# Kernel optimization log

Hardware: AMD Instinct MI355X
Metric: run time of the kernel (lower is better)

## Reference

```python
import jax, jax.numpy as jnp
import numpy as np
import math

B, L, D, H, TOPK = 2, 2048, 1024, 16, 5
DK = D // H
U = min(TOPK * int(np.ceil(np.log1p(L))), L)  # = 40 selected queries


def setup_inputs() -> dict:
    k = jax.random.key(0)
    ks = jax.random.split(k, 9)
    s = 1.0 / math.sqrt(D)  # ~ torch Linear init scale
    return {
        "query": jax.random.normal(ks[0], (B, L, D), jnp.float32),
        "key": jax.random.normal(ks[1], (B, L, D), jnp.float32),
        "value": jax.random.normal(ks[2], (B, L, D), jnp.float32),
        "Wq": jax.random.uniform(ks[3], (D, D), jnp.float32, -s, s),
        "bq": jax.random.uniform(ks[4], (D,), jnp.float32, -s, s),
        "Wk": jax.random.uniform(ks[5], (D, D), jnp.float32, -s, s),
        "bk": jax.random.uniform(ks[6], (D,), jnp.float32, -s, s),
        "Wv": jax.random.uniform(ks[7], (D, D), jnp.float32, -s, s),
        "bv": jax.random.uniform(ks[8], (D,), jnp.float32, -s, s),
    }


def reference(query, key, value, Wq, bq, Wk, bk, Wv, bv):
    # torch Linear: y = x @ W.T + b ; split_heads -> [B, H, L, DK]
    def split(x):
        return x.reshape(B, L, H, DK).transpose(0, 2, 1, 3)

    Q = split(query @ Wq.T + bq)
    K = split(key @ Wk.T + bk)
    V = split(value @ Wv.T + bv)

    # Full score matrix [B,H,L,L]; used only for the sparsity measure M
    # (original's Q_K_sample actually uses full K; sampling is dead code).
    scores_full = jnp.einsum('bhqd,bhkd->bhqk', Q, K)
    M = scores_full.max(axis=-1) - scores_full.mean(axis=-1)  # [B,H,L]

    _, M_top = jax.lax.top_k(M, U)  # [B,H,U] (torch uses sorted=False; set identical)

    Q_red = jnp.take_along_axis(Q, M_top[..., None], axis=2)  # [B,H,U,DK]
    attn_scores = jnp.einsum('bhqd,bhkd->bhqk', Q_red, K) / math.sqrt(DK)

    # default causal mask rows gathered at the selected query positions
    causal = jnp.triu(jnp.ones((L, L), jnp.float32), 1)  # [L_Q, L_K]
    attn_scores = attn_scores + causal[M_top] * (-1e9)   # [B,H,U,L]

    attn_probs = jax.nn.softmax(attn_scores, axis=-1)
    attn = jnp.einsum('bhql,bhld->bqhd', attn_probs, V).reshape(B, U, D)
    return attn, attn_probs
```

## Files before the change

### kernel.cpp

```cpp
#include <hip/hip_runtime.h>
#include <hip/hip_bf16.h>

#define BB 2
#define LL 2048
#define DD 1024
#define HH 16
#define DK 64
#define UU 40
#define BH (BB*HH)

typedef unsigned short u16;
typedef float f32x4 __attribute__((ext_vector_type(4)));
typedef short s16x8 __attribute__((ext_vector_type(8)));

__device__ inline float b2f_r8(u16 x) {
    union { unsigned short u; __hip_bfloat16 b; } c; c.u = x;
    return __bfloat162float(c.b);
}
__device__ inline float ldf_r8(const void* p, size_t i, int isF) {
    return isF ? ((const float*)p)[i] : b2f_r8(((const u16*)p)[i]);
}
__device__ inline f32x4 ld4_r8(const void* p, size_t i, int isF) {
    if (isF) return *(const f32x4*)((const float*)p + i);
    ushort4 v = *(const ushort4*)((const u16*)p + i);
    f32x4 r;
    r[0] = b2f_r8(v.x); r[1] = b2f_r8(v.y); r[2] = b2f_r8(v.z); r[3] = b2f_r8(v.w);
    return r;
}
__device__ inline void cvt2_r8(float x, u16& h, u16& l) {
    union { __hip_bfloat16 b; u16 u; } ch, cl;
    ch.b = __float2bfloat16(x);
    float hf = __bfloat162float(ch.b);
    cl.b = __float2bfloat16(x - hf);
    h = ch.u; l = cl.u;
}

__global__ __launch_bounds__(256) void detect_dtype_r8(const u16* __restrict__ q,
                                                       int* __restrict__ flag) {
    __shared__ float red[256];
    int tid = threadIdx.x;
    float mx = 0.f;
    for (int i = tid; i < 4096; i += 256) {
        float v = fabsf(b2f_r8(q[i]));
        if (!(v < 1e30f)) v = 1e38f;
        mx = fmaxf(mx, v);
    }
    red[tid] = mx; __syncthreads();
    for (int s = 128; s > 0; s >>= 1) {
        if (tid < s) red[tid] = fmaxf(red[tid], red[tid + s]);
        __syncthreads();
    }
    if (tid == 0) *flag = (red[0] > 1e20f) ? 1 : 0;
}

#define PAD 132

__global__ __launch_bounds__(256) void proj_f4_r13(
    const void* __restrict__ key, const void* __restrict__ query,
    const void* __restrict__ Wk, const void* __restrict__ Wq,
    const void* __restrict__ bk, const void* __restrict__ bq,
    float* __restrict__ Kf, float* __restrict__ Qf,
    const int* __restrict__ flag)
{
    __shared__ float sX[32 * PAD];
    __shared__ float sW[32 * 68];
    int tid = threadIdx.x;
    int n0 = blockIdx.x * 128, f0 = blockIdx.y * 64, z = blockIdx.z;
    const void* X    = z ? query : key;
    const void* W    = z ? Wq    : Wk;
    const void* bias = z ? bq    : bk;
    float* out       = z ? Qf    : Kf;
    int isF = *flag;
    int tx = tid & 15, ty = tid >> 4;

    float acc[8][4];
#pragma unroll
    for (int a = 0; a < 8; ++a)
#pragma unroll
        for (int c = 0; c < 4; ++c) acc[a][c] = 0.f;

    for (int kc = 0; kc < 32; ++kc) {
        __syncthreads();
#pragma unroll
        for (int it = 0; it < 4; ++it) {
            int row = 64 * (it & 1) + (tid >> 2);
            int d4 = (tid & 3) | ((it >> 1) << 2);
            f32x4 v = ld4_r8(X, (size_t)(n0 + row) * DD + kc * 32 + d4 * 4, isF);
#pragma unroll
            for (int cc = 0; cc < 4; ++cc)
                sX[(4 * d4 + cc) * PAD + row] = v[cc];
        }
#pragma unroll
        for (int it = 0; it < 2; ++it) {
            int row = tid >> 2;
            int d4 = (tid & 3) | (it << 2);
            f32x4 v = ld4_r8(W, (size_t)(f0 + row) * DD + kc * 32 + d4 * 4, isF);
#pragma unroll
            for (int cc = 0; cc < 4; ++cc)
                sW[(4 * d4 + cc) * 68 + row] = v[cc];
        }
        __syncthreads();
        for (int d = 0; d < 32; ++d) {
            const f32x4 xa = *(const f32x4*)(&sX[d * PAD + ty * 4]);
            const f32x4 xb = *(const f32x4*)(&sX[d * PAD + 64 + ty * 4]);
            const f32x4 wa = *(const f32x4*)(&sW[d * 68 + tx * 4]);
            float xv[8] = {xa[0], xa[1], xa[2], xa[3], xb[0], xb[1], xb[2], xb[3]};
#pragma unroll
            for (int a = 0; a < 8; ++a)
#pragma unroll
                for (int c = 0; c < 4; ++c)
                    acc[a][c] = fmaf(xv[a], wa[c], acc[a][c]);
        }
    }
#pragma unroll
    for (int a = 0; a < 8; ++a) {
        int n = n0 + (a >> 2) * 64 + ty * 4 + (a & 3);
        int b = n >> 11, l = n & (LL - 1);
#pragma unroll
        for (int c = 0; c < 4; ++c) {
            int f = f0 + tx * 4 + c;
            int h = f >> 6, dk = f & 63;
            out[((size_t)(b * HH + h) * LL + l) * DK + dk] =
                acc[a][c] + ldf_r8(bias, (size_t)f, isF);
        }
    }
}

#define LDK 72
__global__ __launch_bounds__(256) void proj_mfma_v_r9(
    const void* __restrict__ X, const void* __restrict__ W,
    const void* __restrict__ bias, float* __restrict__ out,
    const int* __restrict__ flag)
{
    __shared__ u16 Ahi[128 * LDK];
    __shared__ u16 Alo[128 * LDK];
    __shared__ u16 Bhi[128 * LDK];
    __shared__ u16 Blo[128 * LDK];
    int tid = threadIdx.x;
    int n0 = blockIdx.x * 128, f0 = blockIdx.y * 128;
    int isF = *flag;
    int lane = tid & 63, w = tid >> 6, wr = w >> 1, wc = w & 1;

    f32x4 acc[4][4] = {};

    for (int kc = 0; kc < 16; ++kc) {
        __syncthreads();
#pragma unroll
        for (int it = 0; it < 16; ++it) {
            int i = it * 256 + tid;
            int isB = i >> 11, j = i & 2047;
            int row = j >> 4, c = (j & 15) << 2;
            f32x4 v = ld4_r8(isB ? W : X, (size_t)((isB ? f0 : n0) + row) * DD + kc * 64 + c, isF);
            u16* hh = isB ? Bhi : Ahi;
            u16* ll = isB ? Blo : Alo;
            ushort4 h4, l4;
            cvt2_r8(v[0], h4.x, l4.x);
            cvt2_r8(v[1], h4.y, l4.y);
            cvt2_r8(v[2], h4.z, l4.z);
            cvt2_r8(v[3], h4.w, l4.w);
            *(ushort4*)&hh[row * LDK + c] = h4;
            *(ushort4*)&ll[row * LDK + c] = l4;
        }
        __syncthreads();
#pragma unroll
        for (int kk = 0; kk < 2; ++kk) {
            int koff = kk * 32 + (lane >> 4) * 8;
            s16x8 ah[4], al[4];
#pragma unroll
            for (int mi = 0; mi < 4; ++mi) {
                int r = wr * 64 + mi * 16 + (lane & 15);
                ah[mi] = *(const s16x8*)&Ahi[r * LDK + koff];
                al[mi] = *(const s16x8*)&Alo[r * LDK + koff];
            }
#pragma unroll
            for (int ni = 0; ni < 4; ++ni) {
                int r = wc * 64 + ni * 16 + (lane & 15);
                s16x8 bh = *(const s16x8*)&Bhi[r * LDK + koff];
                s16x8 bl = *(const s16x8*)&Blo[r * LDK + koff];
#pragma unroll
                for (int mi = 0; mi < 4; ++mi) {
                    acc[mi][ni] = __builtin_amdgcn_mfma_f32_16x16x32_bf16(ah[mi], bh, acc[mi][ni], 0, 0, 0);
                    acc[mi][ni] = __builtin_amdgcn_mfma_f32_16x16x32_bf16(al[mi], bh, acc[mi][ni], 0, 0, 0);
                    acc[mi][ni] = __builtin_amdgcn_mfma_f32_16x16x32_bf16(ah[mi], bl, acc[mi][ni], 0, 0, 0);
                }
            }
        }
    }

#pragma unroll
    for (int ni = 0; ni < 4; ++ni) {
        int f = f0 + wc * 64 + ni * 16 + (lane & 15);
        float bb = ldf_r8(bias, (size_t)f, isF);
        int h = f >> 6, dk = f & 63;
#pragma unroll
        for (int mi = 0; mi < 4; ++mi) {
            int nbase = n0 + wr * 64 + mi * 16 + ((lane >> 4) << 2);
#pragma unroll
            for (int j2 = 0; j2 < 4; ++j2) {
                int n = nbase + j2, b = n >> 11, l = n & (LL - 1);
                out[((size_t)(b * HH + h) * LL + l) * DK + dk] = acc[mi][ni][j2] + bb;
            }
        }
    }
}

__global__ __launch_bounds__(256) void kbar_r8(
    const float* __restrict__ Kf, double* __restrict__ Kbar)
{
    __shared__ double red[256];
    int bh = blockIdx.x, tid = threadIdx.x;
    int d = tid & 63, seg = tid >> 6;
    double s = 0;
    for (int l = seg * 512; l < seg * 512 + 512; ++l)
        s += (double)Kf[((size_t)bh * LL + l) * DK + d];
    red[tid] = s; __syncthreads();
    if (tid < 128) red[tid] += red[tid + 128];
    __syncthreads();
    if (tid < 64) Kbar[(size_t)bh * DK + d] = (red[tid] + red[tid + 64]) * (1.0 / (double)LL);
}

#define QT 64
__global__ __launch_bounds__(256) void stats_max_r13(
    const float* __restrict__ Qf, const float* __restrict__ Kf,
    const double* __restrict__ Kbar, double* __restrict__ Mv)
{
    __shared__ float sQ[64 * 68];
    __shared__ float sK[64 * 68];
    __shared__ float rowmax[QT];
    int tid = threadIdx.x;
    int q0 = blockIdx.x * QT, bh = blockIdx.y;
    int tx = tid & 15, ty = tid >> 4;

    {
        const float* src = Qf + ((size_t)bh * LL + q0) * DK;
#pragma unroll
        for (int it = 0; it < 4; ++it) {
            int row = tid >> 2;
            int d4 = (tid & 3) | (it << 2);
            f32x4 v = *(const f32x4*)(src + (size_t)row * DK + d4 * 4);
#pragma unroll
            for (int cc = 0; cc < 4; ++cc)
                sQ[(4 * d4 + cc) * 68 + row] = v[cc];
        }
    }
    float rmax4[4];
#pragma unroll
    for (int a = 0; a < 4; ++a) rmax4[a] = -INFINITY;

    const float* kbase = Kf + (size_t)bh * LL * DK;
    for (int kc = 0; kc < 32; ++kc) {
        __syncthreads();
#pragma unroll
        for (int it = 0; it < 4; ++it) {
            int row = tid >> 2;
            int d4 = (tid & 3) | (it << 2);
            f32x4 v = *(const f32x4*)(kbase + (size_t)(kc * 64 + row) * DK + d4 * 4);
#pragma unroll
            for (int cc = 0; cc < 4; ++cc)
                sK[(4 * d4 + cc) * 68 + row] = v[cc];
        }
        __syncthreads();
        float acc[4][4];
#pragma unroll
        for (int a = 0; a < 4; ++a)
#pragma unroll
            for (int c = 0; c < 4; ++c) acc[a][c] = 0.f;
        for (int d = 0; d < 64; ++d) {
            const f32x4 qa = *(const f32x4*)(&sQ[d * 68 + ty * 4]);
            const f32x4 ka = *(const f32x4*)(&sK[d * 68 + tx * 4]);
#pragma unroll
            for (int a = 0; a < 4; ++a)
#pragma unroll
                for (int c = 0; c < 4; ++c)
                    acc[a][c] = fmaf(qa[a], ka[c], acc[a][c]);
        }
#pragma unroll
        for (int a = 0; a < 4; ++a)
#pragma unroll
            for (int c = 0; c < 4; ++c) rmax4[a] = fmaxf(rmax4[a], acc[a][c]);
    }
#pragma unroll
    for (int a = 0; a < 4; ++a) {
        float v = rmax4[a];
        v = fmaxf(v, __shfl_xor(v, 1));
        v = fmaxf(v, __shfl_xor(v, 2));
        v = fmaxf(v, __shfl_xor(v, 4));
        v = fmaxf(v, __shfl_xor(v, 8));
        rmax4[a] = v;
    }
    if (tx == 0) {
#pragma unroll
        for (int a = 0; a < 4; ++a)
            rowmax[ty * 4 + a] = rmax4[a];
    }
    __syncthreads();
    if (tid < QT) {
        const double* kb = Kbar + (size_t)bh * DK;
        double s = 0;
#pragma unroll
        for (int d = 0; d < 64; ++d) s += (double)sQ[d * 68 + tid] * kb[d];
        Mv[(size_t)bh * LL + q0 + tid] = (double)rowmax[tid] - s;
    }
}

__global__ __launch_bounds__(64) void topk_wave_r10(
    const double* __restrict__ Mv, int* __restrict__ sel)
{
    int bh = blockIdx.x, lane = threadIdx.x;
    double v[32];
#pragma unroll
    for (int t = 0; t < 32; ++t) v[t] = Mv[(size_t)bh * LL + t * 64 + lane];
    for (int u = 0; u < UU; ++u) {
        double bv = -1e301; int bi = LL;
#pragma unroll
        for (int t = 0; t < 32; ++t) {
            double x = v[t]; int j = t * 64 + lane;
            if (x > bv || (x == bv && j < bi)) { bv = x; bi = j; }
        }
#pragma unroll
        for (int off = 1; off < 64; off <<= 1) {
            double ov = __shfl_xor(bv, off); int oi = __shfl_xor(bi, off);
            if (ov > bv || (ov == bv && oi < bi)) { bv = ov; bi = oi; }
        }
        if ((bi & 63) == lane) {
            int ts = bi >> 6;
#pragma unroll
            for (int t = 0; t < 32; ++t)
                if (t == ts) v[t] = -1e302;
        }
        if (lane == 0) sel[bh * UU + u] = bi;
    }
}

__global__ __launch_bounds__(256) void scores_r15(
    const float* __restrict__ Qf, const float* __restrict__ Kf,
    const int* __restrict__ sel, float* __restrict__ S)
{
    __shared__ float sK[128 * 68];
    __shared__ float qsm[40 * 68];
    __shared__ int qpos[UU];
    int lq = blockIdx.x, bh = blockIdx.y, tid = threadIdx.x;
    int l0 = lq * 128;
    if (tid < UU) qpos[tid] = sel[bh * UU + tid];
    __syncthreads();
    for (int i = tid; i < 640; i += 256) {
        int u = i >> 4, c4 = i & 15;
        *(f32x4*)&qsm[u * 68 + c4 * 4] =
            *(const f32x4*)&Qf[((size_t)bh * LL + qpos[u]) * DK + c4 * 4];
    }
#pragma unroll
    for (int it = 0; it < 8; ++it) {
        int idx = it * 256 + tid;
        int l = idx >> 4, d4 = idx & 15;
        *(f32x4*)&sK[l * 68 + d4 * 4] =
            *(const f32x4*)&Kf[((size_t)bh * LL + l0 + l) * DK + d4 * 4];
    }
    __syncthreads();
    int gu = tid >> 5, lt = tid & 31;
    float acc[5][4];
#pragma unroll
    for (int ui = 0; ui < 5; ++ui)
#pragma unroll
        for (int li = 0; li < 4; ++li) acc[ui][li] = 0.f;
    for (int d16 = 0; d16 < 16; ++d16) {
        f32x4 qf[5], kf[4];
#pragma unroll
        for (int ui = 0; ui < 5; ++ui)
            qf[ui] = *(const f32x4*)&qsm[(gu + 8 * ui) * 68 + d16 * 4];
#pragma unroll
        for (int li = 0; li < 4; ++li)
            kf[li] = *(const f32x4*)&sK[(lt + 32 * li) * 68 + d16 * 4];
#pragma unroll
        for (int ui = 0; ui < 5; ++ui)
#pragma unroll
            for (int li = 0; li < 4; ++li)
#pragma unroll
                for (int c = 0; c < 4; ++c)
                    acc[ui][li] = fmaf(qf[ui][c], kf[li][c], acc[ui][li]);
    }
#pragma unroll
    for (int ui = 0; ui < 5; ++ui) {
        int u = gu + 8 * ui;
        int qp = qpos[u];
#pragma unroll
        for (int li = 0; li < 4; ++li) {
            int l = l0 + lt + 32 * li;
            float s = acc[ui][li] * 0.125f;
            if (l > qp) s -= 1e9f;
            S[((size_t)bh * UU + u) * LL + l] = s;
        }
    }
}

__global__ __launch_bounds__(256) void softmax_r12(
    const float* __restrict__ S, float* __restrict__ probsOut)
{
    __shared__ float red[256];
    int u = blockIdx.x, bh = blockIdx.y, tid = threadIdx.x;
    size_t rowo = ((size_t)bh * UU + u) * LL;
    float sloc[8];
    float lmax = -INFINITY;
#pragma unroll
    for (int c = 0; c < 8; ++c) {
        sloc[c] = S[rowo + c * 256 + tid];
        lmax = fmaxf(lmax, sloc[c]);
    }
    red[tid] = lmax; __syncthreads();
    for (int s2 = 128; s2 > 0; s2 >>= 1) {
        if (tid < s2) red[tid] = fmaxf(red[tid], red[tid + s2]);
        __syncthreads();
    }
    float mval = red[0];
    __syncthreads();
    float lsum = 0.f;
#pragma unroll
    for (int c = 0; c < 8; ++c) { sloc[c] = expf(sloc[c] - mval); lsum += sloc[c]; }
    red[tid] = lsum; __syncthreads();
    for (int s2 = 128; s2 > 0; s2 >>= 1) {
        if (tid < s2) red[tid] += red[tid + s2];
        __syncthreads();
    }
    float inv = 1.0f / red[0];
#pragma unroll
    for (int c = 0; c < 8; ++c)
        probsOut[rowo + c * 256 + tid] = sloc[c] * inv;
}

__global__ __launch_bounds__(256) void pv_r15(
    const float* __restrict__ probsOut, const float* __restrict__ Vf,
    float* __restrict__ part)
{
    __shared__ float pP[20 * 256];
    int lq = blockIdx.x, bh = blockIdx.y, ug2 = blockIdx.z, tid = threadIdx.x;
    int l0 = lq * 256;
#pragma unroll
    for (int it = 0; it < 5; ++it) {
        int idx = it * 256 + tid;
        int ur = idx >> 6, l4 = idx & 63;
        *(f32x4*)&pP[ur * 256 + l4 * 4] =
            *(const f32x4*)&probsOut[((size_t)bh * UU + ug2 * 20 + ur) * LL + l0 + l4 * 4];
    }
    __syncthreads();
    int dk = tid & 63, ug = tid >> 6;
    const float* vb = Vf + ((size_t)bh * LL + l0) * DK + dk;
    float acc[5];
#pragma unroll
    for (int j = 0; j < 5; ++j) acc[j] = 0.f;
    for (int l4 = 0; l4 < 64; ++l4) {
        float vv0 = vb[(size_t)(l4 * 4 + 0) * DK];
        float vv1 = vb[(size_t)(l4 * 4 + 1) * DK];
        float vv2 = vb[(size_t)(l4 * 4 + 2) * DK];
        float vv3 = vb[(size_t)(l4 * 4 + 3) * DK];
#pragma unroll
        for (int j = 0; j < 5; ++j) {
            const f32x4 p4 = *(const f32x4*)&pP[(ug * 5 + j) * 256 + l4 * 4];
            acc[j] = fmaf(p4[0], vv0, acc[j]);
            acc[j] = fmaf(p4[1], vv1, acc[j]);
            acc[j] = fmaf(p4[2], vv2, acc[j]);
            acc[j] = fmaf(p4[3], vv3, acc[j]);
        }
    }
#pragma unroll
    for (int j = 0; j < 5; ++j) {
        int u = ug2 * 20 + ug * 5 + j;
        part[(((size_t)bh * 8 + lq) * UU + u) * DK + dk] = acc[j];
    }
}

__global__ __launch_bounds__(64) void pvred_r12(
    const float* __restrict__ part, float* __restrict__ attnOut)
{
    int u = blockIdx.x, bh = blockIdx.y, dk = threadIdx.x;
    int b = bh >> 4, h = bh & 15;
    float s = 0.f;
#pragma unroll
    for (int lq = 0; lq < 8; ++lq)
        s += part[(((size_t)bh * 8 + lq) * UU + u) * DK + dk];
    attnOut[((size_t)b * UU + u) * DD + h * DK + dk] = s;
}

extern "C" void kernel_launch(void* const* d_in, const int* in_sizes, int n_in,
                              void* d_out, int out_size, void* d_ws, size_t ws_size,
                              hipStream_t stream) {
    (void)in_sizes; (void)n_in; (void)out_size; (void)ws_size;
    const void* query = d_in[0];
    const void* key   = d_in[1];
    const void* value = d_in[2];
    const void* Wq    = d_in[3];
    const void* bq    = d_in[4];
    const void* Wk    = d_in[5];
    const void* bk    = d_in[6];
    const void* Wv    = d_in[7];
    const void* bv    = d_in[8];

    char* w = (char*)d_ws;
    const size_t NE = (size_t)BB * HH * LL * DK;
    float* Kf  = (float*)w;  w += NE * 4;
    float* Vf  = (float*)w;  w += NE * 4;
    float* Qf  = (float*)w;  w += NE * 4;
    double* Mv = (double*)w; w += (size_t)BH * LL * 8;
    double* Kbar = (double*)w; w += (size_t)BH * DK * 8;
    int* sel   = (int*)w;    w += (size_t)BH * UU * 4;
    int* flag  = (int*)w;    w += 64;
    float* S    = (float*)w; w += (size_t)BH * UU * LL * 4;
    float* part = (float*)w; w += (size_t)BH * 8 * UU * DK * 4;

    float* attnOut  = (float*)d_out;
    float* probsOut = attnOut + (size_t)BB * UU * DD;

    dim3 blk(256);
    detect_dtype_r8<<<1, blk, 0, stream>>>((const u16*)query, flag);
    proj_f4_r13<<<dim3(32, 16, 2), blk, 0, stream>>>(key, query, Wk, Wq, bk, bq,
                                                     Kf, Qf, flag);
    proj_mfma_v_r9<<<dim3(32, 8), blk, 0, stream>>>(value, Wv, bv, Vf, flag);
    kbar_r8<<<32, blk, 0, stream>>>(Kf, Kbar);
    stats_max_r13<<<dim3(LL / QT, 32), blk, 0, stream>>>(Qf, Kf, Kbar, Mv);
    topk_wave_r10<<<32, dim3(64), 0, stream>>>(Mv, sel);
    scores_r15<<<dim3(16, 32), blk, 0, stream>>>(Qf, Kf, sel, S);
    softmax_r12<<<dim3(UU, 32), blk, 0, stream>>>(S, probsOut);
    pv_r15<<<dim3(8, 32, 2), blk, 0, stream>>>(probsOut, Vf, part);
    pvred_r12<<<dim3(UU, 32), dim3(64), 0, stream>>>(part, attnOut);
}
```

Baseline: 912.2 us.

## Pre-convert Wv to bf16 hi/lo, shrink V-proj tile, enlarge stats query tile

```diff
diff --git a/kernel.cpp b/kernel.cpp
--- a/kernel.cpp
+++ b/kernel.cpp
@@ -126,49 +126,70 @@
     }
 }
 
+__global__ __launch_bounds__(256) void preconvW_r16(
+    const void* __restrict__ Wv, u16* __restrict__ Whi, u16* __restrict__ Wlo,
+    const int* __restrict__ flag)
+{
+    int isF = *flag;
+    size_t i = ((size_t)blockIdx.x * 256 + threadIdx.x) * 4;
+    f32x4 v = ld4_r8(Wv, i, isF);
+    ushort4 h4, l4;
+    cvt2_r8(v[0], h4.x, l4.x);
+    cvt2_r8(v[1], h4.y, l4.y);
+    cvt2_r8(v[2], h4.z, l4.z);
+    cvt2_r8(v[3], h4.w, l4.w);
+    *(ushort4*)&Whi[i] = h4;
+    *(ushort4*)&Wlo[i] = l4;
+}
+
 #define LDK 72
-__global__ __launch_bounds__(256) void proj_mfma_v_r9(
-    const void* __restrict__ X, const void* __restrict__ W,
-    const void* __restrict__ bias, float* __restrict__ out,
-    const int* __restrict__ flag)
-{
-    __shared__ u16 Ahi[128 * LDK];
-    __shared__ u16 Alo[128 * LDK];
+__global__ __launch_bounds__(256) void proj_mfma_v_r16(
+    const void* __restrict__ X, const u16* __restrict__ Whi,
+    const u16* __restrict__ Wlo, const void* __restrict__ bias,
+    float* __restrict__ out, const int* __restrict__ flag)
+{
+    __shared__ u16 Ahi[64 * LDK];
+    __shared__ u16 Alo[64 * LDK];
     __shared__ u16 Bhi[128 * LDK];
     __shared__ u16 Blo[128 * LDK];
     int tid = threadIdx.x;
-    int n0 = blockIdx.x * 128, f0 = blockIdx.y * 128;
+    int n0 = blockIdx.x * 64, f0 = blockIdx.y * 128;
     int isF = *flag;
     int lane = tid & 63, w = tid >> 6, wr = w >> 1, wc = w & 1;
 
-    f32x4 acc[4][4] = {};
+    f32x4 acc[2][4] = {};
 
     for (int kc = 0; kc < 16; ++kc) {
         __syncthreads();
 #pragma unroll
-        for (int it = 0; it < 16; ++it) {
+        for (int it = 0; it < 4; ++it) {
             int i = it * 256 + tid;
-            int isB = i >> 11, j = i & 2047;
-            int row = j >> 4, c = (j & 15) << 2;
-            f32x4 v = ld4_r8(isB ? W : X, (size_t)((isB ? f0 : n0) + row) * DD + kc * 64 + c, isF);
-            u16* hh = isB ? Bhi : Ahi;
-            u16* ll = isB ? Blo : Alo;
+            int row = i >> 4, c = (i & 15) << 2;
+            f32x4 v = ld4_r8(X, (size_t)(n0 + row) * DD + kc * 64 + c, isF);
             ushort4 h4, l4;
             cvt2_r8(v[0], h4.x, l4.x);
             cvt2_r8(v[1], h4.y, l4.y);
             cvt2_r8(v[2], h4.z, l4.z);
             cvt2_r8(v[3], h4.w, l4.w);
-            *(ushort4*)&hh[row * LDK + c] = h4;
-            *(ushort4*)&ll[row * LDK + c] = l4;
+            *(ushort4*)&Ahi[row * LDK + c] = h4;
+            *(ushort4*)&Alo[row * LDK + c] = l4;
+        }
+#pragma unroll
+        for (int it = 0; it < 8; ++it) {
+            int i = it * 256 + tid;
+            int row = i >> 4, c = (i & 15) << 2;
+            size_t go = (size_t)(f0 + row) * DD + kc * 64 + c;
+            *(ushort4*)&Bhi[row * LDK + c] = *(const ushort4*)&Whi[go];
+            *(ushort4*)&Blo[row * LDK + c] = *(const ushort4*)&Wlo[go];
         }
         __syncthreads();
 #pragma unroll
         for (int kk = 0; kk < 2; ++kk) {
             int koff = kk * 32 + (lane >> 4) * 8;
-            s16x8 ah[4], al[4];
-#pragma unroll
-            for (int mi = 0; mi < 4; ++mi) {
-                int r = wr * 64 + mi * 16 + (lane & 15);
+            s16x8 ah[2], al[2];
+#pragma unroll
+            for (int mi = 0; mi < 2; ++mi) {
+                int r = wr * 32 + mi * 16 + (lane & 15);
                 ah[mi] = *(const s16x8*)&Ahi[r * LDK + koff];
                 al[mi] = *(const s16x8*)&Alo[r * LDK + koff];
             }
@@ -178,7 +199,7 @@
                 s16x8 bh = *(const s16x8*)&Bhi[r * LDK + koff];
                 s16x8 bl = *(const s16x8*)&Blo[r * LDK + koff];
 #pragma unroll
-                for (int mi = 0; mi < 4; ++mi) {
+                for (int mi = 0; mi < 2; ++mi) {
                     acc[mi][ni] = __builtin_amdgcn_mfma_f32_16x16x32_bf16(ah[mi], bh, acc[mi][ni], 0, 0, 0);
                     acc[mi][ni] = __builtin_amdgcn_mfma_f32_16x16x32_bf16(al[mi], bh, acc[mi][ni], 0, 0, 0);
                     acc[mi][ni] = __builtin_amdgcn_mfma_f32_16x16x32_bf16(ah[mi], bl, acc[mi][ni], 0, 0, 0);
@@ -193,8 +214,8 @@
         float bb = ldf_r8(bias, (size_t)f, isF);
         int h = f >> 6, dk = f & 63;
 #pragma unroll
-        for (int mi = 0; mi < 4; ++mi) {
-            int nbase = n0 + wr * 64 + mi * 16 + ((lane >> 4) << 2);
+        for (int mi = 0; mi < 2; ++mi) {
+            int nbase = n0 + wr * 32 + mi * 16 + ((lane >> 4) << 2);
 #pragma unroll
             for (int j2 = 0; j2 < 4; ++j2) {
                 int n = nbase + j2, b = n >> 11, l = n & (LL - 1);
@@ -219,33 +240,33 @@
     if (tid < 64) Kbar[(size_t)bh * DK + d] = (red[tid] + red[tid + 64]) * (1.0 / (double)LL);
 }
 
-#define QT 64
-__global__ __launch_bounds__(256) void stats_max_r13(
+#define QTS 128
+__global__ __launch_bounds__(256) void stats_max_r12(
     const float* __restrict__ Qf, const float* __restrict__ Kf,
     const double* __restrict__ Kbar, double* __restrict__ Mv)
 {
-    __shared__ float sQ[64 * 68];
+    __shared__ float sQ[64 * PAD];
     __shared__ float sK[64 * 68];
-    __shared__ float rowmax[QT];
+    __shared__ float rowmax[QTS];
     int tid = threadIdx.x;
-    int q0 = blockIdx.x * QT, bh = blockIdx.y;
+    int q0 = blockIdx.x * QTS, bh = blockIdx.y;
     int tx = tid & 15, ty = tid >> 4;
 
     {
         const float* src = Qf + ((size_t)bh * LL + q0) * DK;
 #pragma unroll
-        for (int it = 0; it < 4; ++it) {
-            int row = tid >> 2;
-            int d4 = (tid & 3) | (it << 2);
+        for (int it = 0; it < 8; ++it) {
+            int row = 64 * (it & 1) + (tid >> 2);
+            int d4 = (tid & 3) | ((it >> 1) << 2);
             f32x4 v = *(const f32x4*)(src + (size_t)row * DK + d4 * 4);
 #pragma unroll
             for (int cc = 0; cc < 4; ++cc)
-                sQ[(4 * d4 + cc) * 68 + row] = v[cc];
-        }
-    }
-    float rmax4[4];
-#pragma unroll
-    for (int a = 0; a < 4; ++a) rmax4[a] = -INFINITY;
+                sQ[(4 * d4 + cc) * PAD + row] = v[cc];
+        }
+    }
+    float rmax8[8];
+#pragma unroll
+    for (int a = 0; a < 8; ++a) rmax8[a] = -INFINITY;
 
     const float* kbase = Kf + (size_t)bh * LL * DK;
     for (int kc = 0; kc < 32; ++kc) {
@@ -260,45 +281,49 @@
                 sK[(4 * d4 + cc) * 68 + row] = v[cc];
         }
         __syncthreads();
-        float acc[4][4];
-#pragma unroll
-        for (int a = 0; a < 4; ++a)
+        float acc[8][4];
+#pragma unroll
+        for (int a = 0; a < 8; ++a)
 #pragma unroll
             for (int c = 0; c < 4; ++c) acc[a][c] = 0.f;
         for (int d = 0; d < 64; ++d) {
-            const f32x4 qa = *(const f32x4*)(&sQ[d * 68 + ty * 4]);
+            const f32x4 qa = *(const f32x4*)(&sQ[d * PAD + ty * 4]);
+            const f32x4 qb = *(const f32x4*)(&sQ[d * PAD + 64 + ty * 4]);
             const f32x4 ka = *(const f32x4*)(&sK[d * 68 + tx * 4]);
-#pragma unroll
-            for (int a = 0; a < 4; ++a)
+            float qv[8] = {qa[0], qa[1], qa[2], qa[3], qb[0], qb[1], qb[2], qb[3]};
+#pragma unroll
+            for (int a = 0; a < 8; ++a)
 #pragma unroll
                 for (int c = 0; c < 4; ++c)
-                    acc[a][c] = fmaf(qa[a], ka[c], acc[a][c]);
-        }
-#pragma unroll
-        for (int a = 0; a < 4; ++a)
-#pragma unroll
-            for (int c = 0; c < 4; ++c) rmax4[a] = fmaxf(rmax4[a], acc[a][c]);
-    }
-#pragma unroll
-    for (int a = 0; a < 4; ++a) {
-        float v = rmax4[a];
+                    acc[a][c] = fmaf(qv[a], ka[c], acc[a][c]);
+        }
+#pragma unroll
+        for (int a = 0; a < 8; ++a)
+#pragma unroll
+            for (int c = 0; c < 4; ++c) rmax8[a] = fmaxf(rmax8[a], acc[a][c]);
+    }
+#pragma unroll
+    for (int a = 0; a < 8; ++a) {
+        float v = rmax8[a];
         v = fmaxf(v, __shfl_xor(v, 1));
         v = fmaxf(v, __shfl_xor(v, 2));
         v = fmaxf(v, __shfl_xor(v, 4));
         v = fmaxf(v, __shfl_xor(v, 8));
-        rmax4[a] = v;
+        rmax8[a] = v;
     }
     if (tx == 0) {
 #pragma unroll
-        for (int a = 0; a < 4; ++a)
-            rowmax[ty * 4 + a] = rmax4[a];
+        for (int a = 0; a < 8; ++a) {
+            int row = ty * 4 + (a & 3) + (a >> 2) * 64;
+            rowmax[row] = rmax8[a];
+        }
     }
     __syncthreads();
-    if (tid < QT) {
+    if (tid < QTS) {
         const double* kb = Kbar + (size_t)bh * DK;
         double s = 0;
 #pragma unroll
-        for (int d = 0; d < 64; ++d) s += (double)sQ[d * 68 + tid] * kb[d];
+        for (int d = 0; d < 64; ++d) s += (double)sQ[d * PAD + tid] * kb[d];
         Mv[(size_t)bh * LL + q0 + tid] = (double)rowmax[tid] - s;
     }
 }
@@ -504,17 +529,20 @@
     int* flag  = (int*)w;    w += 64;
     float* S    = (float*)w; w += (size_t)BH * UU * LL * 4;
     float* part = (float*)w; w += (size_t)BH * 8 * UU * DK * 4;
+    u16* Whi = (u16*)w;      w += (size_t)DD * DD * 2;
+    u16* Wlo = (u16*)w;      w += (size_t)DD * DD * 2;
 
     float* attnOut  = (float*)d_out;
     float* probsOut = attnOut + (size_t)BB * UU * DD;
 
     dim3 blk(256);
     detect_dtype_r8<<<1, blk, 0, stream>>>((const u16*)query, flag);
+    preconvW_r16<<<1024, blk, 0, stream>>>(Wv, Whi, Wlo, flag);
     proj_f4_r13<<<dim3(32, 16, 2), blk, 0, stream>>>(key, query, Wk, Wq, bk, bq,
                                                      Kf, Qf, flag);
-    proj_mfma_v_r9<<<dim3(32, 8), blk, 0, stream>>>(value, Wv, bv, Vf, flag);
+    proj_mfma_v_r16<<<dim3(64, 8), blk, 0, stream>>>(value, Whi, Wlo, bv, Vf, flag);
     kbar_r8<<<32, blk, 0, stream>>>(Kf, Kbar);
-    stats_max_r13<<<dim3(LL / QT, 32), blk, 0, stream>>>(Qf, Kf, Kbar, Mv);
+    stats_max_r12<<<dim3(LL / QTS, 32), blk, 0, stream>>>(Qf, Kf, Kbar, Mv);
     topk_wave_r10<<<32, dim3(64), 0, stream>>>(Mv, sel);
     scores_r15<<<dim3(16, 32), blk, 0, stream>>>(Qf, Kf, sel, S);
     softmax_r12<<<dim3(UU, 32), blk, 0, stream>>>(S, probsOut);
```

Result: faster. 821.1 us (-10.0%).
